# Kernel optimization log

Measured on AMD Instinct MI355X. Metric: run time of the kernel, lower is better.

## Reference

```python
import jax, jax.numpy as jnp
import numpy as np


def setup_inputs() -> dict:
    key = jax.random.key(0)
    k1, k2, k3 = jax.random.split(key, 3)
    B, S, H, Dk = 4, 1024, 16, 4
    E = H * Dk
    return {
        "x": jax.random.normal(k1, (B, S, E), dtype=jnp.float32),
        "theta": jax.random.normal(k2, (Dk,), dtype=jnp.float32),  # heads[0] RY params, shared by all heads (bug in source reproduced)
        "W": jax.random.normal(k3, (E, E), dtype=jnp.float32) / np.sqrt(E),
        "b": jnp.zeros((E,), dtype=jnp.float32),
    }


def reference(x, theta, W, b):
    # x: [B, S, E], E = H * 4
    B, S, E = x.shape
    Dk = 4
    H = E // Dk
    inv_sqrt_dk = 1.0 / np.float32(np.sqrt(Dk))

    # 4-qubit circuit per token/head, no entangling gates -> each wire independent:
    #   |0> --RX(x_i)--RY(theta_i)--  <PauliZ> = cos(theta_i) * cos(x_i)
    # (exact closed form of the torchquantum statevector simulation)
    # chunk along embed dim == reshape [B, S, H, Dk]
    proj = jnp.cos(x.reshape(B, S, H, Dk)) * jnp.cos(theta)  # theta broadcasts over wires
    proj = proj.transpose(0, 2, 1, 3)  # [B, H, S, Dk]

    scores = jnp.einsum('bhsd,bhtd->bhst', proj, proj) * inv_sqrt_dk  # [B, H, S, S]
    attn = jax.nn.softmax(scores, axis=-1)  # dropout = identity in eval mode
    out = jnp.einsum('bhst,bhtd->bhsd', attn, proj)  # [B, H, S, Dk]

    out = out.transpose(0, 2, 1, 3).reshape(B, S, E)  # [B, S, E]
    return out @ W.T + b
```

## Files before the change

### kernel.cpp

```cpp
#include <hip/hip_runtime.h>
#include <hip/hip_bf16.h>

#define SQ 1024
#define HH 16
#define DK 4
#define EE 64

using short8 = __attribute__((ext_vector_type(8))) short;
using f32x4  = __attribute__((ext_vector_type(4))) float;
using us4    = __attribute__((ext_vector_type(4))) unsigned short;
using us8    = __attribute__((ext_vector_type(8))) unsigned short;
using u32x4  = __attribute__((ext_vector_type(4))) unsigned;

static __device__ inline unsigned short f2bf(float f) {
  return __builtin_bit_cast(unsigned short, __float2bfloat16(f));
}

static __device__ inline unsigned trunc_pk_bf16(float lo, float hi) {
  return __builtin_amdgcn_perm(__builtin_bit_cast(unsigned, hi),
                               __builtin_bit_cast(unsigned, lo),
                               0x07060302u);
}

__global__ __launch_bounds__(512) void qattn_mfma(
    const float* __restrict__ x, const float* __restrict__ theta,
    float* __restrict__ y) {
  const int tid = threadIdx.x;
  const int quarter = blockIdx.x & 3;
  const int bh = blockIdx.x >> 2;
  const int hd = bh & (HH - 1);
  const int b = bh >> 4;

  __shared__ __align__(16) unsigned short afrag[32][16][8];
  __shared__ __align__(16) unsigned short vfrag[32][4][5][8];
  __shared__ __align__(16) unsigned short qfrag[256][4];
  __shared__ __align__(16) unsigned short zslot[8];

  const float4 th = *reinterpret_cast<const float4*>(theta);
  const float ct[4] = {__cosf(th.x), __cosf(th.y), __cosf(th.z), __cosf(th.w)};
  const float sc = 0.5f * 1.4426950408889634f;
  const int q_lo = quarter * 256;

  if (tid < 8) zslot[tid] = 0;
#pragma unroll
  for (int k = 0; k < 2; ++k) {
    const int e = tid + k * 512;
    vfrag[e >> 5][(e >> 3) & 3][4][e & 7] = 0x3F80;
  }

  const float* xb = x + ((size_t)b * SQ) * EE + hd * DK;
#pragma unroll
  for (int k = 0; k < 2; ++k) {
    const int t = tid + k * 512;
    const float4 v = *reinterpret_cast<const float4*>(xb + (size_t)t * EE);
    const float p[4] = {__cosf(v.x) * ct[0], __cosf(v.y) * ct[1],
                        __cosf(v.z) * ct[2], __cosf(v.w) * ct[3]};
    unsigned short pb[4], qb[4];
#pragma unroll
    for (int d = 0; d < 4; ++d) {
      pb[d] = f2bf(p[d]);
      qb[d] = f2bf(p[d] * sc);
    }
    const int c = t >> 5, tl = t & 31, hq = tl >> 3, j = tl & 7;
    *reinterpret_cast<us4*>(&afrag[c][4 * hq + (j & 3)][(j >= 4) ? 4 : 0]) =
        (us4){pb[0], pb[1], pb[2], pb[3]};
#pragma unroll
    for (int nn = 0; nn < 4; ++nn) vfrag[c][hq][nn][j] = pb[nn];
    const int ql = t - q_lo;
    if ((unsigned)ql < 256u)
      *reinterpret_cast<us4*>(&qfrag[ql][0]) = (us4){qb[0], qb[1], qb[2], qb[3]};
  }
  __syncthreads();

  const int lane = tid & 63;
  const int wid = tid >> 6;
  const int n = lane & 15, hg = lane >> 4;

  short8 qf0 = {0, 0, 0, 0, 0, 0, 0, 0}, qf1 = qf0;
  {
    const unsigned short* qa =
        (lane < 16) ? &qfrag[wid * 32 + n][0] : &zslot[0];
    const unsigned short* qb2 =
        (lane < 16) ? &qfrag[wid * 32 + 16 + n][0] : &zslot[0];
    const us4 ta = *reinterpret_cast<const us4*>(qa);
    const us4 tb = *reinterpret_cast<const us4*>(qb2);
#pragma unroll
    for (int i = 0; i < 4; ++i) { qf0[i] = (short)ta[i]; qf1[i] = (short)tb[i]; }
  }

  const unsigned short* aptr = (lane < 16) ? &afrag[0][n][0] : &zslot[0];
  const int astep = (lane < 16) ? 128 : 0;
  const unsigned short* vptr = (n <= 4) ? &vfrag[0][hg][n][0] : &zslot[0];
  const int vstep = (n <= 4) ? 160 : 0;

  f32x4 acc0 = {0.f, 0.f, 0.f, 0.f}, acc1 = acc0;
  const float csh = 0.0056245491938781f;
  const f32x4 cc = {csh, csh, csh, csh};

#pragma unroll 2
  for (int c = 0; c < 32; ++c) {
    const us8 av = *reinterpret_cast<const us8*>(aptr + c * astep);
    const short8 A1 = {(short)av[0], (short)av[1], (short)av[2], (short)av[3],
                       0, 0, 0, 0};
    const short8 A2 = {(short)av[4], (short)av[5], (short)av[6], (short)av[7],
                       0, 0, 0, 0};
    const f32x4 s1a = __builtin_amdgcn_mfma_f32_16x16x32_bf16(A1, qf0, cc, 0, 0, 0);
    const f32x4 s2a = __builtin_amdgcn_mfma_f32_16x16x32_bf16(A2, qf0, cc, 0, 0, 0);
    const f32x4 s1b = __builtin_amdgcn_mfma_f32_16x16x32_bf16(A1, qf1, cc, 0, 0, 0);
    const f32x4 s2b = __builtin_amdgcn_mfma_f32_16x16x32_bf16(A2, qf1, cc, 0, 0, 0);

    u32x4 p0, p1;
    p0[0] = trunc_pk_bf16(__builtin_amdgcn_exp2f(s1a[0]),
                          __builtin_amdgcn_exp2f(s1a[1]));
    p0[1] = trunc_pk_bf16(__builtin_amdgcn_exp2f(s1a[2]),
                          __builtin_amdgcn_exp2f(s1a[3]));
    p0[2] = trunc_pk_bf16(__builtin_amdgcn_exp2f(s2a[0]),
                          __builtin_amdgcn_exp2f(s2a[1]));
    p0[3] = trunc_pk_bf16(__builtin_amdgcn_exp2f(s2a[2]),
                          __builtin_amdgcn_exp2f(s2a[3]));
    p1[0] = trunc_pk_bf16(__builtin_amdgcn_exp2f(s1b[0]),
                          __builtin_amdgcn_exp2f(s1b[1]));
    p1[1] = trunc_pk_bf16(__builtin_amdgcn_exp2f(s1b[2]),
                          __builtin_amdgcn_exp2f(s1b[3]));
    p1[2] = trunc_pk_bf16(__builtin_amdgcn_exp2f(s2b[0]),
                          __builtin_amdgcn_exp2f(s2b[1]));
    p1[3] = trunc_pk_bf16(__builtin_amdgcn_exp2f(s2b[2]),
                          __builtin_amdgcn_exp2f(s2b[3]));
    const short8 PA0 = __builtin_bit_cast(short8, p0);
    const short8 PA1 = __builtin_bit_cast(short8, p1);

    const us8 vv = *reinterpret_cast<const us8*>(vptr + c * vstep);
    const short8 VB = __builtin_bit_cast(short8, vv);
    acc0 = __builtin_amdgcn_mfma_f32_16x16x32_bf16(PA0, VB, acc0, 0, 0, 0);
    acc1 = __builtin_amdgcn_mfma_f32_16x16x32_bf16(PA1, VB, acc1, 0, 0, 0);
  }

#pragma unroll
  for (int half = 0; half < 2; ++half) {
    const f32x4 acc = half ? acc1 : acc0;
    const int qbase = q_lo + wid * 32 + half * 16;
#pragma unroll
    for (int r = 0; r < 4; ++r) {
      const float den = __shfl(acc[r], (lane & 48) | 4, 64);
      const float val = acc[r] * (1.0f / den);
      if (n < 4) {
        y[((size_t)(b * SQ + qbase + 4 * hg + r)) * EE + hd * DK + n] = val;
      }
    }
  }
}

__global__ __launch_bounds__(256) void proj_kernel(
    const float* __restrict__ y, const float* __restrict__ W,
    const float* __restrict__ bias, float* __restrict__ out) {
  const int tid = threadIdx.x;
  __shared__ float Wt[EE][68];
  __shared__ float yt[16][68];

  const float4* W4 = reinterpret_cast<const float4*>(W);
#pragma unroll
  for (int k = 0; k < 4; ++k) {
    const int i4 = tid + k * 256;
    const float4 w = W4[i4];
    const int e = i4 >> 4;
    const int j0 = (i4 & 15) * 4;
    Wt[j0 + 0][e] = w.x; Wt[j0 + 1][e] = w.y;
    Wt[j0 + 2][e] = w.z; Wt[j0 + 3][e] = w.w;
  }
  const size_t tok0 = (size_t)blockIdx.x * 16;
  {
    const float4 v = reinterpret_cast<const float4*>(y + tok0 * EE)[tid];
    *reinterpret_cast<float4*>(&yt[tid >> 4][(tid & 15) * 4]) = v;
  }
  __syncthreads();

  const int t = tid >> 4;
  const int eg = tid & 15;
  const int e0 = eg * 4;
  f32x4 acc = *reinterpret_cast<const f32x4*>(bias + e0);
#pragma unroll
  for (int jq = 0; jq < 16; ++jq) {
    const f32x4 yv = *reinterpret_cast<const f32x4*>(&yt[t][jq * 4]);
    const f32x4 w0 = *reinterpret_cast<const f32x4*>(&Wt[jq * 4 + 0][e0]);
    const f32x4 w1 = *reinterpret_cast<const f32x4*>(&Wt[jq * 4 + 1][e0]);
    const f32x4 w2 = *reinterpret_cast<const f32x4*>(&Wt[jq * 4 + 2][e0]);
    const f32x4 w3 = *reinterpret_cast<const f32x4*>(&Wt[jq * 4 + 3][e0]);
    acc += yv[0] * w0 + yv[1] * w1 + yv[2] * w2 + yv[3] * w3;
  }
  *reinterpret_cast<f32x4*>(&out[((size_t)tok0 + t) * EE + e0]) = acc;
}

extern "C" void kernel_launch(void* const* d_in, const int* in_sizes, int n_in,
                              void* d_out, int out_size, void* d_ws, size_t ws_size,
                              hipStream_t stream) {
  const float* x     = (const float*)d_in[0];
  const float* theta = (const float*)d_in[1];
  const float* W     = (const float*)d_in[2];
  const float* bias  = (const float*)d_in[3];
  float* out = (float*)d_out;
  float* y   = (float*)d_ws;

  qattn_mfma<<<256, 512, 0, stream>>>(x, theta, y);
  proj_kernel<<<256, 256, 0, stream>>>(y, W, bias, out);
}
```

Measured before the change: 20.23 us.

## Split attention key loop across two wave groups with LDS reduction

Doubles the attention block to 1024 threads. Each half of the waves processes half of the key chunks, and the partial accumulators are summed through shared memory before normalization and store. Token preprocessing now runs one token per thread instead of a two-iteration loop. This shortens the serial MFMA/exp chain per wave to raise latency hiding, at the cost of extra barriers, an LDS exchange, and higher register pressure under the 1024-thread launch bound.

```diff
diff --git a/kernel.cpp b/kernel.cpp
--- a/kernel.cpp
+++ b/kernel.cpp
@@ -22,7 +22,7 @@
                                0x07060302u);
 }
 
-__global__ __launch_bounds__(512) void qattn_mfma(
+__global__ __launch_bounds__(1024) void qattn_mfma(
     const float* __restrict__ x, const float* __restrict__ theta,
     float* __restrict__ y) {
   const int tid = threadIdx.x;
@@ -31,10 +31,15 @@
   const int hd = bh & (HH - 1);
   const int b = bh >> 4;
 
-  __shared__ __align__(16) unsigned short afrag[32][16][8];
-  __shared__ __align__(16) unsigned short vfrag[32][4][5][8];
-  __shared__ __align__(16) unsigned short qfrag[256][4];
-  __shared__ __align__(16) unsigned short zslot[8];
+  __shared__ __align__(16) unsigned char smem[20496];
+  typedef unsigned short afrag_t[16][8];
+  typedef unsigned short vfrag_t[4][5][8];
+  afrag_t* afrag = reinterpret_cast<afrag_t*>(smem);
+  vfrag_t* vfrag = reinterpret_cast<vfrag_t*>(smem + 8192);
+  unsigned short (*qfrag)[4] =
+      reinterpret_cast<unsigned short (*)[4]>(smem + 18432);
+  unsigned short* zslot = reinterpret_cast<unsigned short*>(smem + 20480);
+  f32x4* pex = reinterpret_cast<f32x4*>(smem);
 
   const float4 th = *reinterpret_cast<const float4*>(theta);
   const float ct[4] = {__cosf(th.x), __cosf(th.y), __cosf(th.z), __cosf(th.w)};
@@ -42,16 +47,11 @@
   const int q_lo = quarter * 256;
 
   if (tid < 8) zslot[tid] = 0;
-#pragma unroll
-  for (int k = 0; k < 2; ++k) {
-    const int e = tid + k * 512;
-    vfrag[e >> 5][(e >> 3) & 3][4][e & 7] = 0x3F80;
-  }
+  vfrag[tid >> 5][(tid >> 3) & 3][4][tid & 7] = 0x3F80;
 
   const float* xb = x + ((size_t)b * SQ) * EE + hd * DK;
-#pragma unroll
-  for (int k = 0; k < 2; ++k) {
-    const int t = tid + k * 512;
+  {
+    const int t = tid;
     const float4 v = *reinterpret_cast<const float4*>(xb + (size_t)t * EE);
     const float p[4] = {__cosf(v.x) * ct[0], __cosf(v.y) * ct[1],
                         __cosf(v.z) * ct[2], __cosf(v.w) * ct[3]};
@@ -73,7 +73,9 @@
   __syncthreads();
 
   const int lane = tid & 63;
-  const int wid = tid >> 6;
+  const int wid16 = tid >> 6;
+  const int wid = wid16 & 7;
+  const int khalf = wid16 >> 3;
   const int n = lane & 15, hg = lane >> 4;
 
   short8 qf0 = {0, 0, 0, 0, 0, 0, 0, 0}, qf1 = qf0;
@@ -97,8 +99,9 @@
   const float csh = 0.0056245491938781f;
   const f32x4 cc = {csh, csh, csh, csh};
 
+  const int c0 = khalf * 16;
 #pragma unroll 2
-  for (int c = 0; c < 32; ++c) {
+  for (int c = c0; c < c0 + 16; ++c) {
     const us8 av = *reinterpret_cast<const us8*>(aptr + c * astep);
     const short8 A1 = {(short)av[0], (short)av[1], (short)av[2], (short)av[3],
                        0, 0, 0, 0};
@@ -135,16 +138,29 @@
     acc1 = __builtin_amdgcn_mfma_f32_16x16x32_bf16(PA1, VB, acc1, 0, 0, 0);
   }
 
-#pragma unroll
-  for (int half = 0; half < 2; ++half) {
-    const f32x4 acc = half ? acc1 : acc0;
-    const int qbase = q_lo + wid * 32 + half * 16;
-#pragma unroll
-    for (int r = 0; r < 4; ++r) {
-      const float den = __shfl(acc[r], (lane & 48) | 4, 64);
-      const float val = acc[r] * (1.0f / den);
-      if (n < 4) {
-        y[((size_t)(b * SQ + qbase + 4 * hg + r)) * EE + hd * DK + n] = val;
+  __syncthreads();
+  if (khalf == 1) {
+    const int p = wid * 64 + lane;
+    pex[p * 2 + 0] = acc0;
+    pex[p * 2 + 1] = acc1;
+  }
+  __syncthreads();
+  if (khalf == 0) {
+    const int p = wid * 64 + lane;
+    acc0 += pex[p * 2 + 0];
+    acc1 += pex[p * 2 + 1];
+
+#pragma unroll
+    for (int half = 0; half < 2; ++half) {
+      const f32x4 acc = half ? acc1 : acc0;
+      const int qbase = q_lo + wid * 32 + half * 16;
+#pragma unroll
+      for (int r = 0; r < 4; ++r) {
+        const float den = __shfl(acc[r], (lane & 48) | 4, 64);
+        const float val = acc[r] * (1.0f / den);
+        if (n < 4) {
+          y[((size_t)(b * SQ + qbase + 4 * hg + r)) * EE + hd * DK + n] = val;
+        }
       }
     }
   }
@@ -200,6 +216,6 @@
   float* out = (float*)d_out;
   float* y   = (float*)d_ws;
 
-  qattn_mfma<<<256, 512, 0, stream>>>(x, theta, y);
+  qattn_mfma<<<256, 1024, 0, stream>>>(x, theta, y);
   proj_kernel<<<256, 256, 0, stream>>>(y, W, bias, out);
 }
```

Result: faster. 19.55 us (-3.4%).
